# Kernel tuning notes

Measured on AMD Instinct MI355X. Metric: run time of the kernel, lower is better.

Reference implementation:

```python
import jax, jax.numpy as jnp
import numpy as np

TOP_K = 8
NORM_TOPK_PROB = True


def setup_inputs() -> dict:
    key = jax.random.key(0)
    k1, k2 = jax.random.split(key)
    T, H, E = 16384, 4096, 64  # tokens, hidden_dim, num_experts
    hidden_states = jax.random.normal(k1, (T, H), dtype=jnp.float32)
    weight = jax.random.normal(k2, (E, H), dtype=jnp.float32) * 0.02
    return {"hidden_states": hidden_states, "weight": weight}


def reference(hidden_states, weight):
    H = weight.shape[1]
    x = hidden_states.reshape(-1, H)                      # [T, H]
    router_logits = jnp.einsum("th,eh->te", x, weight)    # [T, E]
    routing_weights = jax.nn.softmax(router_logits.astype(jnp.float32), axis=-1)
    router_top_value, router_indices = jax.lax.top_k(routing_weights, TOP_K)  # [T, k]
    if NORM_TOPK_PROB:
        router_top_value = router_top_value / jnp.sum(router_top_value, axis=-1, keepdims=True)
    router_scores = router_top_value.astype(routing_weights.dtype)
    return router_logits, router_scores, router_indices
```

## Files before the change

### kernel.cpp

```cpp
#include <hip/hip_runtime.h>
#include <math.h>

#define T_TOK  16384
#define HID    4096
#define NEXP   64
#define KSPLIT 4
#define KRANGE (HID / KSPLIT)
#define NCHUNK (KRANGE / 32)

typedef __attribute__((ext_vector_type(8))) short short8;
typedef __attribute__((ext_vector_type(4))) float float4v;

#define PART_ELEMS ((size_t)KSPLIT * T_TOK * NEXP)
#define WHALF      ((size_t)NEXP * HID)

__device__ __forceinline__ unsigned short rne_bf16(float f) {
  unsigned u = __float_as_uint(f);
  unsigned r = u + 0x7FFFu + ((u >> 16) & 1u);
  return (unsigned short)(r >> 16);
}
__device__ __forceinline__ float bf16_f(unsigned short h) {
  return __uint_as_float(((unsigned)h) << 16);
}

__global__ void w_convert3(const float* __restrict__ w,
                           unsigned short* __restrict__ wh,
                           unsigned short* __restrict__ wm,
                           unsigned short* __restrict__ wl) {
  int t = blockIdx.x * 256 + threadIdx.x;
#pragma unroll
  for (int j = 0; j < 4; ++j) {
    int idx = t + j * 65536;
    float f = w[idx];
    unsigned short h = rne_bf16(f);
    float r1 = f - bf16_f(h);
    unsigned short m = rne_bf16(r1);
    float r2 = r1 - bf16_f(m);
    wh[idx] = h; wm[idx] = m; wl[idx] = rne_bf16(r2);
  }
}

__global__ __launch_bounds__(256, 2)
void router_gemm(const float* __restrict__ x,
                 const unsigned short* __restrict__ wh,
                 const unsigned short* __restrict__ wm,
                 const unsigned short* __restrict__ wl,
                 float* __restrict__ partial) {
  const int lane = threadIdx.x & 63;
  const int wid  = threadIdx.x >> 6;
  const int W    = blockIdx.x * 4 + wid;
  const int ks   = W & (KSPLIT - 1);
  const int t0   = (W >> 2) * 32;
  const int r    = lane & 15;
  const int q    = lane >> 4;
  const int k0   = ks * KRANGE + q * 8;

  const float* pa0 = x + (size_t)(t0 + r) * HID + k0;
  const float* pa1 = pa0 + (size_t)16 * HID;
  const unsigned short* pb[3];
  pb[0] = wh + (size_t)r * HID + k0;
  pb[1] = wm + (size_t)r * HID + k0;
  pb[2] = wl + (size_t)r * HID + k0;

  float4v acc[2][4];
#pragma unroll
  for (int m = 0; m < 2; ++m)
#pragma unroll
    for (int n = 0; n < 4; ++n) acc[m][n] = (float4v)(0.f);

  float4 araw[4][2][2];
  short8 ah[2], am_[2], al[2];
  short8 Bb[2][2][3];

#define LOADA(buf, c) do {                                                   \
    const int _o = (c) * 32;                                                 \
    araw[buf][0][0] = *(const float4*)(pa0 + _o);                            \
    araw[buf][0][1] = *(const float4*)(pa0 + _o + 4);                        \
    araw[buf][1][0] = *(const float4*)(pa1 + _o);                            \
    araw[buf][1][1] = *(const float4*)(pa1 + _o + 4);                        \
  } while (0)

#define LOADB(half, c) do {                                                  \
    const int _o = (c) * 32;                                                 \
    _Pragma("unroll")                                                        \
    for (int _nl = 0; _nl < 2; ++_nl) {                                      \
      const size_t _nb = (size_t)((half) * 2 + _nl) * 16 * HID + _o;         \
      _Pragma("unroll")                                                      \
      for (int _s = 0; _s < 3; ++_s)                                         \
        Bb[half][_nl][_s] = *(const short8*)(pb[_s] + _nb);                  \
    }                                                                        \
  } while (0)

#define SPLITA(buf) do {                                                     \
    _Pragma("unroll")                                                        \
    for (int _m = 0; _m < 2; ++_m) {                                         \
      const float4 _v0 = araw[buf][_m][0], _v1 = araw[buf][_m][1];           \
      float _f[8] = {_v0.x,_v0.y,_v0.z,_v0.w,_v1.x,_v1.y,_v1.z,_v1.w};       \
      _Pragma("unroll")                                                      \
      for (int _j = 0; _j < 8; ++_j) {                                       \
        unsigned short _h = rne_bf16(_f[_j]);                                \
        float _r1 = _f[_j] - bf16_f(_h);                                     \
        unsigned short _mm = rne_bf16(_r1);                                  \
        float _r2 = _r1 - bf16_f(_mm);                                       \
        ah[_m][_j] = (short)_h; am_[_m][_j] = (short)_mm;                    \
        al[_m][_j] = (short)rne_bf16(_r2);                                   \
      }                                                                      \
    }                                                                        \
  } while (0)

#define MFMAH(half) do {                                                     \
    _Pragma("unroll")                                                        \
    for (int _nl = 0; _nl < 2; ++_nl) {                                      \
      const int _n = (half) * 2 + _nl;                                       \
      const short8 _BH = Bb[half][_nl][0];                                   \
      const short8 _BM = Bb[half][_nl][1];                                   \
      const short8 _BL = Bb[half][_nl][2];                                   \
      _Pragma("unroll")                                                      \
      for (int _m = 0; _m < 2; ++_m) {                                       \
        float4v _a = acc[_m][_n];                                            \
        _a = __builtin_amdgcn_mfma_f32_16x16x32_bf16(al[_m],  _BH, _a,0,0,0);\
        _a = __builtin_amdgcn_mfma_f32_16x16x32_bf16(ah[_m],  _BL, _a,0,0,0);\
        _a = __builtin_amdgcn_mfma_f32_16x16x32_bf16(am_[_m], _BM, _a,0,0,0);\
        _a = __builtin_amdgcn_mfma_f32_16x16x32_bf16(am_[_m], _BH, _a,0,0,0);\
        _a = __builtin_amdgcn_mfma_f32_16x16x32_bf16(ah[_m],  _BM, _a,0,0,0);\
        _a = __builtin_amdgcn_mfma_f32_16x16x32_bf16(ah[_m],  _BH, _a,0,0,0);\
        acc[_m][_n] = _a;                                                    \
      }                                                                      \
    }                                                                        \
  } while (0)

  LOADA(0, 0); LOADA(1, 1);
  LOADB(0, 0);
  for (int cc = 0; cc < NCHUNK; cc += 4) {
    if (cc + 2 < NCHUNK) LOADA(2, cc + 2);
    SPLITA(0); LOADB(1, cc);     MFMAH(0);
    LOADB(0, cc + 1);            MFMAH(1);

    if (cc + 3 < NCHUNK) LOADA(3, cc + 3);
    SPLITA(1); LOADB(1, cc + 1); MFMAH(0);
    LOADB(0, cc + 2);            MFMAH(1);

    if (cc + 4 < NCHUNK) LOADA(0, cc + 4);
    SPLITA(2); LOADB(1, cc + 2); MFMAH(0);
    LOADB(0, cc + 3);            MFMAH(1);

    if (cc + 5 < NCHUNK) LOADA(1, cc + 5);
    SPLITA(3); LOADB(1, cc + 3); MFMAH(0);
    if (cc + 4 < NCHUNK) LOADB(0, cc + 4);
    MFMAH(1);
  }
#undef LOADA
#undef LOADB
#undef SPLITA
#undef MFMAH

  float* po = partial + ((size_t)ks * T_TOK + t0) * NEXP;
#pragma unroll
  for (int m = 0; m < 2; ++m)
#pragma unroll
    for (int n = 0; n < 4; ++n)
#pragma unroll
      for (int rr = 0; rr < 4; ++rr)
        po[(size_t)(m * 16 + q * 4 + rr) * NEXP + n * 16 + r] = acc[m][n][rr];
}

__global__ __launch_bounds__(256)
void router_topk(const float* __restrict__ partial,
                 float* __restrict__ logits_out,
                 float* __restrict__ scores_out,
                 float* __restrict__ idx_out) {
  const int lane = threadIdx.x & 63;
  const int wid  = threadIdx.x >> 6;
  const int t    = blockIdx.x * 4 + wid;

  float ps[KSPLIT];
#pragma unroll
  for (int s = 0; s < KSPLIT; ++s)
    ps[s] = partial[((size_t)s * T_TOK + t) * NEXP + lane];
  float l = (ps[0] + ps[1]) + (ps[2] + ps[3]);
  logits_out[(size_t)t * NEXP + lane] = l;

  float m = l;
#pragma unroll
  for (int off = 32; off >= 1; off >>= 1)
    m = fmaxf(m, __shfl_xor(m, off, 64));
  float p = __expf(l - m);

  float v = l;
  float myscore = 0.f, myidx = 0.f, ssum = 0.f;
#pragma unroll
  for (int k = 0; k < 8; ++k) {
    float bv = v; int bi = lane;
#pragma unroll
    for (int off = 32; off >= 1; off >>= 1) {
      float ov = __shfl_xor(bv, off, 64);
      int   oi = __shfl_xor(bi, off, 64);
      if (ov > bv || (ov == bv && oi < bi)) { bv = ov; bi = oi; }
    }
    float pw = __shfl(p, bi, 64);
    ssum += pw;
    if (lane == k)  { myscore = pw; myidx = (float)bi; }
    if (lane == bi) v = -INFINITY;
  }
  if (lane < 8) {
    scores_out[(size_t)t * 8 + lane] = myscore / ssum;
    idx_out[(size_t)t * 8 + lane]    = myidx;
  }
}

extern "C" void kernel_launch(void* const* d_in, const int* in_sizes, int n_in,
                              void* d_out, int out_size, void* d_ws, size_t ws_size,
                              hipStream_t stream) {
  const float* x = (const float*)d_in[0];
  const float* w = (const float*)d_in[1];
  float* out    = (float*)d_out;
  float* logits = out;
  float* scores = out + (size_t)T_TOK * NEXP;
  float* idxo   = scores + (size_t)T_TOK * 8;

  float* partial = (float*)d_ws;
  unsigned short* wh = (unsigned short*)((char*)d_ws + PART_ELEMS * sizeof(float));
  unsigned short* wm = wh + WHALF;
  unsigned short* wl = wm + WHALF;

  hipLaunchKernelGGL(w_convert3, dim3(256), dim3(256), 0, stream, w, wh, wm, wl);
  hipLaunchKernelGGL(router_gemm, dim3(2048 / 4), dim3(256), 0, stream,
                     x, wh, wm, wl, partial);
  hipLaunchKernelGGL(router_topk, dim3(T_TOK / 4), dim3(256), 0, stream,
                     partial, logits, scores, idxo);
}
```

Before: 457.3 us.

## Template K-split to 8, shrink register pipeline, rework top-k with per-lane octets

The GEMM is templated on the K-split factor and uses 8 splits when the workspace is large enough, which doubles the number of waves over the same work. Launch bounds go from 2 to 4 blocks per SM, and A double-buffering replaces quad-buffering to cut register use. The top-k kernel now handles 8 tokens per wave, each lane holding 8 logits, with local argmax plus 3-step shuffles, and it applies softmax only to the 8 winners. The cost is twice the partial-sum traffic and a bigger reduction in the top-k step.

```diff
diff --git a/kernel.cpp b/kernel.cpp
--- a/kernel.cpp
+++ b/kernel.cpp
@@ -1,18 +1,13 @@
 #include <hip/hip_runtime.h>
 #include <math.h>
 
-#define T_TOK  16384
-#define HID    4096
-#define NEXP   64
-#define KSPLIT 4
-#define KRANGE (HID / KSPLIT)
-#define NCHUNK (KRANGE / 32)
+#define T_TOK 16384
+#define HID   4096
+#define NEXP  64
+#define WHALF ((size_t)NEXP * HID)
 
 typedef __attribute__((ext_vector_type(8))) short short8;
 typedef __attribute__((ext_vector_type(4))) float float4v;
-
-#define PART_ELEMS ((size_t)KSPLIT * T_TOK * NEXP)
-#define WHALF      ((size_t)NEXP * HID)
 
 __device__ __forceinline__ unsigned short rne_bf16(float f) {
   unsigned u = __float_as_uint(f);
@@ -40,17 +35,20 @@
   }
 }
 
-__global__ __launch_bounds__(256, 2)
+template <int KS>
+__global__ __launch_bounds__(256, 4)
 void router_gemm(const float* __restrict__ x,
                  const unsigned short* __restrict__ wh,
                  const unsigned short* __restrict__ wm,
                  const unsigned short* __restrict__ wl,
                  float* __restrict__ partial) {
+  constexpr int KRANGE = HID / KS;
+  constexpr int NCH = KRANGE / 32;
   const int lane = threadIdx.x & 63;
   const int wid  = threadIdx.x >> 6;
   const int W    = blockIdx.x * 4 + wid;
-  const int ks   = W & (KSPLIT - 1);
-  const int t0   = (W >> 2) * 32;
+  const int ks   = W & (KS - 1);
+  const int t0   = (W / KS) * 32;
   const int r    = lane & 15;
   const int q    = lane >> 4;
   const int k0   = ks * KRANGE + q * 8;
@@ -68,7 +66,7 @@
 #pragma unroll
     for (int n = 0; n < 4; ++n) acc[m][n] = (float4v)(0.f);
 
-  float4 araw[4][2][2];
+  float4 araw[2][2][2];
   short8 ah[2], am_[2], al[2];
   short8 Bb[2][2][3];
 
@@ -129,24 +127,15 @@
     }                                                                        \
   } while (0)
 
-  LOADA(0, 0); LOADA(1, 1);
+  LOADA(0, 0);
   LOADB(0, 0);
-  for (int cc = 0; cc < NCHUNK; cc += 4) {
-    if (cc + 2 < NCHUNK) LOADA(2, cc + 2);
-    SPLITA(0); LOADB(1, cc);     MFMAH(0);
-    LOADB(0, cc + 1);            MFMAH(1);
-
-    if (cc + 3 < NCHUNK) LOADA(3, cc + 3);
-    SPLITA(1); LOADB(1, cc + 1); MFMAH(0);
-    LOADB(0, cc + 2);            MFMAH(1);
-
-    if (cc + 4 < NCHUNK) LOADA(0, cc + 4);
-    SPLITA(2); LOADB(1, cc + 2); MFMAH(0);
-    LOADB(0, cc + 3);            MFMAH(1);
-
-    if (cc + 5 < NCHUNK) LOADA(1, cc + 5);
-    SPLITA(3); LOADB(1, cc + 3); MFMAH(0);
-    if (cc + 4 < NCHUNK) LOADB(0, cc + 4);
+  for (int c = 0; c < NCH; ++c) {
+    const int cb = c & 1, nb = cb ^ 1;
+    if (c + 1 < NCH) LOADA(nb, c + 1);
+    SPLITA(cb);
+    LOADB(1, c);
+    MFMAH(0);
+    if (c + 1 < NCH) LOADB(0, c + 1);
     MFMAH(1);
   }
 #undef LOADA
@@ -164,6 +153,7 @@
         po[(size_t)(m * 16 + q * 4 + rr) * NEXP + n * 16 + r] = acc[m][n][rr];
 }
 
+template <int KS>
 __global__ __launch_bounds__(256)
 void router_topk(const float* __restrict__ partial,
                  float* __restrict__ logits_out,
@@ -171,41 +161,61 @@
                  float* __restrict__ idx_out) {
   const int lane = threadIdx.x & 63;
   const int wid  = threadIdx.x >> 6;
-  const int t    = blockIdx.x * 4 + wid;
-
-  float ps[KSPLIT];
-#pragma unroll
-  for (int s = 0; s < KSPLIT; ++s)
-    ps[s] = partial[((size_t)s * T_TOK + t) * NEXP + lane];
-  float l = (ps[0] + ps[1]) + (ps[2] + ps[3]);
-  logits_out[(size_t)t * NEXP + lane] = l;
-
-  float m = l;
-#pragma unroll
-  for (int off = 32; off >= 1; off >>= 1)
-    m = fmaxf(m, __shfl_xor(m, off, 64));
-  float p = __expf(l - m);
-
-  float v = l;
-  float myscore = 0.f, myidx = 0.f, ssum = 0.f;
+  const int g    = lane >> 3;
+  const int j    = lane & 7;
+  const int t    = blockIdx.x * 32 + wid * 8 + g;
+
+  const float* pp = partial + (size_t)t * NEXP + j * 8;
+  float4v a0 = (float4v)(0.f), a1 = (float4v)(0.f);
+#pragma unroll
+  for (int s = 0; s < KS; ++s) {
+    const float4v* p4 = (const float4v*)(pp + (size_t)s * T_TOK * NEXP);
+    a0 += p4[0];
+    a1 += p4[1];
+  }
+  float4v* lo = (float4v*)(logits_out + (size_t)t * NEXP + j * 8);
+  lo[0] = a0; lo[1] = a1;
+
+  float v[8] = {a0[0], a0[1], a0[2], a0[3], a1[0], a1[1], a1[2], a1[3]};
+  float lv = v[0]; int li = 0;
+#pragma unroll
+  for (int i = 1; i < 8; ++i) {
+    bool b = v[i] > lv;
+    lv = b ? v[i] : lv; li = b ? i : li;
+  }
+
+  float win_v = 0.f; int win_i = 0;
 #pragma unroll
   for (int k = 0; k < 8; ++k) {
-    float bv = v; int bi = lane;
-#pragma unroll
-    for (int off = 32; off >= 1; off >>= 1) {
+    float bv = lv; int bi = j * 8 + li;
+#pragma unroll
+    for (int off = 1; off <= 4; off <<= 1) {
       float ov = __shfl_xor(bv, off, 64);
       int   oi = __shfl_xor(bi, off, 64);
       if (ov > bv || (ov == bv && oi < bi)) { bv = ov; bi = oi; }
     }
-    float pw = __shfl(p, bi, 64);
-    ssum += pw;
-    if (lane == k)  { myscore = pw; myidx = (float)bi; }
-    if (lane == bi) v = -INFINITY;
-  }
-  if (lane < 8) {
-    scores_out[(size_t)t * 8 + lane] = myscore / ssum;
-    idx_out[(size_t)t * 8 + lane]    = myidx;
-  }
+    if (j == k) { win_v = bv; win_i = bi; }
+    const bool own = (bi >> 3) == j;
+    const int  sl  = bi & 7;
+#pragma unroll
+    for (int i = 0; i < 8; ++i)
+      if (own && sl == i) v[i] = -INFINITY;
+    lv = v[0]; li = 0;
+#pragma unroll
+    for (int i = 1; i < 8; ++i) {
+      bool b = v[i] > lv;
+      lv = b ? v[i] : lv; li = b ? i : li;
+    }
+  }
+
+  float mx = __shfl(win_v, lane & 56, 64);
+  float p  = __expf(win_v - mx);
+  float ssum = p;
+#pragma unroll
+  for (int off = 1; off <= 4; off <<= 1) ssum += __shfl_xor(ssum, off, 64);
+
+  scores_out[(size_t)t * 8 + j] = p / ssum;
+  idx_out[(size_t)t * 8 + j]    = (float)win_i;
 }
 
 extern "C" void kernel_launch(void* const* d_in, const int* in_sizes, int n_in,
@@ -218,14 +228,25 @@
   float* scores = out + (size_t)T_TOK * NEXP;
   float* idxo   = scores + (size_t)T_TOK * 8;
 
+  const size_t need8 = (size_t)8 * T_TOK * NEXP * sizeof(float) + 3 * WHALF * 2;
+  const int KS = (ws_size >= need8) ? 8 : 4;
+
   float* partial = (float*)d_ws;
-  unsigned short* wh = (unsigned short*)((char*)d_ws + PART_ELEMS * sizeof(float));
+  unsigned short* wh = (unsigned short*)((char*)d_ws +
+                        (size_t)KS * T_TOK * NEXP * sizeof(float));
   unsigned short* wm = wh + WHALF;
   unsigned short* wl = wm + WHALF;
 
   hipLaunchKernelGGL(w_convert3, dim3(256), dim3(256), 0, stream, w, wh, wm, wl);
-  hipLaunchKernelGGL(router_gemm, dim3(2048 / 4), dim3(256), 0, stream,
-                     x, wh, wm, wl, partial);
-  hipLaunchKernelGGL(router_topk, dim3(T_TOK / 4), dim3(256), 0, stream,
-                     partial, logits, scores, idxo);
-}
+  if (KS == 8) {
+    hipLaunchKernelGGL((router_gemm<8>), dim3((T_TOK / 32) * 8 / 4), dim3(256),
+                       0, stream, x, wh, wm, wl, partial);
+    hipLaunchKernelGGL((router_topk<8>), dim3(T_TOK / 32), dim3(256),
+                       0, stream, partial, logits, scores, idxo);
+  } else {
+    hipLaunchKernelGGL((router_gemm<4>), dim3((T_TOK / 32) * 4 / 4), dim3(256),
+                       0, stream, x, wh, wm, wl, partial);
+    hipLaunchKernelGGL((router_topk<4>), dim3(T_TOK / 32), dim3(256),
+                       0, stream, partial, logits, scores, idxo);
+  }
+}
```

Result: slower. 520.6 us (+13.8%).
